# Performance work log

Hardware: AMD Instinct MI355X
Metric: run time of the kernel (lower is better)

Reference implementation:

```python
import jax, jax.numpy as jnp
import numpy as np

DIM = 10  # GMM components == feature dim


def _conv(x, w, b):
    y = jax.lax.conv_general_dilated(x, w, window_strides=(1, 1), padding='VALID',
                                     dimension_numbers=('NCHW', 'OIHW', 'NCHW'))
    return y + b[None, :, None, None]


def _gmm(x, centers, raw_mats):
    # x: [B, d]; centers: [K, d]; raw_mats: [K, d, d] with K == d == DIM
    K, d = centers.shape
    I = jnp.eye(d, dtype=x.dtype)
    L = jnp.tril(raw_mats, -1) + I                       # unit lower-triangular [K,d,d]
    root_D = jnp.diagonal(raw_mats, axis1=-2, axis2=-1)  # [K,d]
    D = root_D * root_D + 1e-4
    # Sigma_inv = L^{-T} D^{-1} L^{-1}
    L_inv = jax.scipy.linalg.solve_triangular(L, jnp.broadcast_to(I, L.shape), lower=True)
    Sigma_inv = jnp.einsum('kai,ka,kaj->kij', L_inv, 1.0 / D, L_inv)
    det_scale = jax.lax.rsqrt(jnp.prod(D, axis=-1))      # [K]
    diff = x[:, None, :] - centers[None, :, :]           # [B,K,d]
    dist_sq = jnp.einsum('bkd,kde,bke->bk', diff, Sigma_inv, diff)
    expo = -0.5 * dist_sq
    expo_safe = expo - jnp.max(expo, axis=1, keepdims=True)
    numer = det_scale[None, :] * jnp.exp(expo_safe)
    return numer / jnp.sum(numer, axis=1, keepdims=True)


def setup_inputs() -> dict:
    key = jax.random.key(0)
    ks = jax.random.split(key, 12)
    B = 4096
    x = jax.random.normal(ks[0], (B, 1, 28, 28), dtype=jnp.float32)
    conv1_w = jax.random.normal(ks[1], (32, 1, 3, 3), jnp.float32) * (1.0 / np.sqrt(1 * 9))
    conv1_b = jnp.zeros((32,), jnp.float32)
    conv2_w = jax.random.normal(ks[2], (64, 32, 3, 3), jnp.float32) * (1.0 / np.sqrt(32 * 9))
    conv2_b = jnp.zeros((64,), jnp.float32)
    fc1_w = jax.random.normal(ks[3], (128, 9216), jnp.float32) * (1.0 / np.sqrt(9216))
    fc1_b = jnp.zeros((128,), jnp.float32)
    fc2_w = jax.random.normal(ks[4], (DIM, 128), jnp.float32) * (1.0 / np.sqrt(128))
    fc2_b = jnp.zeros((DIM,), jnp.float32)
    centers = jax.random.normal(ks[5], (DIM, DIM), jnp.float32)
    raw_mats = jax.random.normal(ks[6], (DIM, DIM, DIM), jnp.float32) * 0.1 + jnp.eye(DIM)[None]
    return {'x': x, 'conv1_w': conv1_w, 'conv1_b': conv1_b, 'conv2_w': conv2_w,
            'conv2_b': conv2_b, 'fc1_w': fc1_w, 'fc1_b': fc1_b, 'fc2_w': fc2_w,
            'fc2_b': fc2_b, 'centers': centers, 'raw_mats': raw_mats}


def reference(x, conv1_w, conv1_b, conv2_w, conv2_b, fc1_w, fc1_b, fc2_w, fc2_b, centers, raw_mats):
    h = jax.nn.relu(_conv(x, conv1_w, conv1_b))          # [B,32,26,26]
    h = jax.nn.relu(_conv(h, conv2_w, conv2_b))          # [B,64,24,24]
    h = jax.lax.reduce_window(h, -jnp.inf, jax.lax.max, (1, 1, 2, 2), (1, 1, 2, 2), 'VALID')
    h = h.reshape(h.shape[0], -1)                        # [B,9216] (dropout = identity in eval)
    h = jax.nn.relu(h @ fc1_w.T + fc1_b)
    h = h @ fc2_w.T + fc2_b                              # [B,10]
    return _gmm(h, centers, raw_mats)
```

## Files before the change

### kernel.cpp

```cpp
#include <hip/hip_runtime.h>

typedef _Float16 half_t;
typedef _Float16 half8  __attribute__((ext_vector_type(8)));
typedef _Float16 half2v __attribute__((ext_vector_type(2)));
typedef float    floatx4 __attribute__((ext_vector_type(4)));
typedef float    float2v __attribute__((ext_vector_type(2)));

#define MFMA16(a, b, c) __builtin_amdgcn_mfma_f32_16x16x32_f16((a), (b), (c), 0, 0, 0)

__global__ void k_prep(const float* __restrict__ fw1, half_t* __restrict__ W1h,
                       const float* __restrict__ w2, half_t* __restrict__ W2T,
                       const float* __restrict__ raw, float* __restrict__ Sinv,
                       float* __restrict__ dets) {
    __shared__ float s_raw[1000];
    __shared__ float s_Li[1000];
    __shared__ float s_Dinv[100];
    const int blk = blockIdx.x;
    const int t = threadIdx.x;
    if (blk < 4608) {
        const int i = blk * 256 + t;
        W1h[i] = (half_t)fw1[i];
    } else if (blk < 4680) {
        const int i = (blk - 4608) * 256 + t;
        if (i < 18432) {
            const int tap = i / 2048;
            const int r = i - tap * 2048;
            const int co = r >> 5;
            const int ci = r & 31;
            W2T[i] = (half_t)w2[(co * 32 + ci) * 9 + tap];
        }
    } else {
        for (int i = t; i < 1000; i += 256) s_raw[i] = raw[i];
        __syncthreads();
        if (t < 100) {
            const int k = t / 10;
            const int j = t - k * 10;
            float v[10];
#pragma unroll
            for (int i = 0; i < 10; ++i) {
                float s = (i == j) ? 1.0f : 0.0f;
#pragma unroll
                for (int mm = 0; mm < 10; ++mm)
                    if (mm < i) s -= s_raw[k * 100 + i * 10 + mm] * v[mm];
                v[i] = s;
            }
#pragma unroll
            for (int a = 0; a < 10; ++a) s_Li[k * 100 + a * 10 + j] = v[a];
        } else if (t < 110) {
            const int k = t - 100;
            float prod = 1.0f;
#pragma unroll
            for (int a = 0; a < 10; ++a) {
                const float rd = s_raw[k * 100 + a * 10 + a];
                const float dv = rd * rd + 1e-4f;
                s_Dinv[k * 10 + a] = 1.0f / dv;
                prod *= dv;
            }
            dets[k] = rsqrtf(prod);
        }
        __syncthreads();
        for (int idx = t; idx < 1000; idx += 256) {
            const int k = idx / 100;
            const int r = idx - k * 100;
            const int ii = r / 10;
            const int jj = r - ii * 10;
            float s = 0.0f;
#pragma unroll
            for (int a = 0; a < 10; ++a)
                s += s_Li[k * 100 + a * 10 + ii] * s_Dinv[k * 10 + a] *
                     s_Li[k * 100 + a * 10 + jj];
            Sinv[idx] = s;
        }
    }
}

__global__ __launch_bounds__(256, 3) void k_convs(
    const float* __restrict__ x, const float* __restrict__ w1,
    const float* __restrict__ b1, const float* __restrict__ b2,
    const half_t* __restrict__ W2T, half_t* __restrict__ h2p) {
    __shared__ float s_x[784];
    __shared__ float s_w1[288];
    __shared__ float s_b1[32];
    __shared__ float s_b2[64];
    __shared__ __align__(16) half_t s_h1[688 * 32];

    const int t = threadIdx.x;
    const int b = blockIdx.x;

    for (int i = t; i < 784; i += 256) s_x[i] = x[(size_t)b * 784 + i];
    for (int i = t; i < 288; i += 256) s_w1[i] = w1[i];
    if (t < 32) s_b1[t] = b1[t];
    if (t < 64) s_b2[t] = b2[t];
    if (t < 48) {
        const int qq = t / 12;
        const int pp = 676 + (t - qq * 12);
        half8 z = {0, 0, 0, 0, 0, 0, 0, 0};
        *(half8*)((char*)s_h1 + (qq * 11008 + (pp << 4))) = z;
    }
    __syncthreads();

    const int w = t >> 6;
    const int ln = t & 63;
    const int n16 = ln & 15;
    const int q = ln >> 4;

    {
        float2v wr2[4][9], br2[4];
#pragma unroll
        for (int m = 0; m < 4; ++m) {
            br2[m][0] = s_b1[w * 8 + 2 * m];
            br2[m][1] = s_b1[w * 8 + 2 * m + 1];
#pragma unroll
            for (int k = 0; k < 9; ++k) {
                wr2[m][k][0] = s_w1[(w * 8 + 2 * m) * 9 + k];
                wr2[m][k][1] = s_w1[(w * 8 + 2 * m + 1) * 9 + k];
            }
        }
        for (int p = ln; p < 676; p += 64) {
            const int yy = p / 26;
            const int xx = p - yy * 26;
            float2v a2[4] = {br2[0], br2[1], br2[2], br2[3]};
#pragma unroll
            for (int r = 0; r < 3; ++r)
#pragma unroll
                for (int c = 0; c < 3; ++c) {
                    const float xv = s_x[(yy + r) * 28 + xx + c];
                    const float2v xv2 = {xv, xv};
#pragma unroll
                    for (int m = 0; m < 4; ++m)
                        a2[m] = xv2 * wr2[m][r * 3 + c] + a2[m];
                }
            half8 hv;
#pragma unroll
            for (int m = 0; m < 4; ++m) {
                hv[2 * m] = (half_t)fmaxf(a2[m][0], 0.0f);
                hv[2 * m + 1] = (half_t)fmaxf(a2[m][1], 0.0f);
            }
            *(half8*)((char*)s_h1 + (w * 11008 + (p << 4))) = hv;
        }
    }

    const int cp = w & 1;
    const int st = w >> 1;
    half8 bf[9][2];
#pragma unroll
    for (int tap = 0; tap < 9; ++tap)
#pragma unroll
        for (int cc = 0; cc < 2; ++cc)
            bf[tap][cc] = *(const half8*)(W2T +
                ((tap * 64 + (2 * cp + cc) * 16 + n16) * 32 + q * 8));

    __syncthreads();

#pragma unroll
    for (int tap = 0; tap < 9; ++tap)
#pragma unroll
        for (int cc = 0; cc < 2; ++cc)
            asm volatile("" : "+v"(bf[tap][cc]));

    const char* rp = (const char*)s_h1 + (q * 11008 + ((n16 + 16 * st) << 4));

    const float bb0 = s_b2[cp * 32 + n16];
    const float bb1 = s_b2[cp * 32 + 16 + n16];
    half_t* outp = h2p + (size_t)b * 9216 + (size_t)(cp * 32 + n16) * 144 +
                   8 * st + 2 * q;
    const bool dostore = (st == 0) | (q < 2);

    const floatx4 z4 = {0.f, 0.f, 0.f, 0.f};
    floatx4 sl0[2] = {z4, z4}, sl1[2] = {z4, z4}, sl2[2] = {z4, z4};
    float yb00 = 0.f, yb01 = 0.f, yb10 = 0.f, yb11 = 0.f;

#define RETIRE(YO, AC)                                                        \
    do {                                                                      \
        const float p0 = fmaxf(AC[0][0], AC[0][1]);                           \
        const float p1 = fmaxf(AC[0][2], AC[0][3]);                           \
        const float r0 = fmaxf(AC[1][0], AC[1][1]);                           \
        const float r1 = fmaxf(AC[1][2], AC[1][3]);                           \
        if (((YO) & 1) == 0) {                                                \
            yb00 = p0; yb01 = p1; yb10 = r0; yb11 = r1;                       \
        } else if (dostore) {                                                 \
            half2v h0, h1v;                                                   \
            h0[0] = (half_t)fmaxf(fmaxf(yb00, p0) + bb0, 0.0f);               \
            h0[1] = (half_t)fmaxf(fmaxf(yb01, p1) + bb0, 0.0f);               \
            h1v[0] = (half_t)fmaxf(fmaxf(yb10, r0) + bb1, 0.0f);              \
            h1v[1] = (half_t)fmaxf(fmaxf(yb11, r1) + bb1, 0.0f);              \
            half_t* op = outp + ((YO) >> 1) * 12;                             \
            *(half2v*)(op) = h0;                                              \
            *(half2v*)(op + 2304) = h1v;                                      \
        }                                                                     \
        AC[0] = z4; AC[1] = z4;                                               \
    } while (0)

#define CSTEP(Y_, A0, A1, A2)                                                 \
    do {                                                                      \
        const int y_ = (Y_);                                                  \
        if (y_ < 26) {                                                        \
            const half8 f0 = *(const half8*)(rp);                             \
            const half8 f1 = *(const half8*)(rp + 16);                        \
            const half8 f2 = *(const half8*)(rp + 32);                        \
            if (y_ <= 23) {                 \
                A0[0] = MFMA16(f0, bf[0][0], A0[0]);                          \
                A0[1] = MFMA16(f0, bf[0][1], A0[1]);                          \
                A0[0] = MFMA16(f1, bf[1][0], A0[0]);                          \
                A0[1] = MFMA16(f1, bf[1][1], A0[1]);                          \
                A0[0] = MFMA16(f2, bf[2][0], A0[0]);                          \
                A0[1] = MFMA16(f2, bf[2][1], A0[1]);                          \
            }                                                                 \
            if (y_ >= 1 && y_ <= 24) {    \
                A1[0] = MFMA16(f0, bf[3][0], A1[0]);                          \
                A1[1] = MFMA16(f0, bf[3][1], A1[1]);                          \
                A1[0] = MFMA16(f1, bf[4][0], A1[0]);                          \
                A1[1] = MFMA16(f1, bf[4][1], A1[1]);                          \
                A1[0] = MFMA16(f2, bf[5][0], A1[0]);                          \
                A1[1] = MFMA16(f2, bf[5][1], A1[1]);                          \
            }                                                                 \
            if (y_ >= 2) {   \
                A2[0] = MFMA16(f0, bf[6][0], A2[0]);                          \
                A2[1] = MFMA16(f0, bf[6][1], A2[1]);                          \
                A2[0] = MFMA16(f1, bf[7][0], A2[0]);                          \
                A2[1] = MFMA16(f1, bf[7][1], A2[1]);                          \
                A2[0] = MFMA16(f2, bf[8][0], A2[0]);                          \
                A2[1] = MFMA16(f2, bf[8][1], A2[1]);                          \
                RETIRE(y_ - 2, A2);                                           \
            }                                                                 \
            rp += 416;                                                        \
        }                                                                     \
    } while (0)

    for (int yb = 0; yb < 27; yb += 3) {
        CSTEP(yb + 0, sl0, sl2, sl1);
        CSTEP(yb + 1, sl1, sl0, sl2);
        CSTEP(yb + 2, sl2, sl1, sl0);
    }
#undef CSTEP
#undef RETIRE
}

__global__ __launch_bounds__(256) void k_fc1(const half_t* __restrict__ A,
                                             const half_t* __restrict__ W,
                                             half_t* __restrict__ part) {
    const int t = threadIdx.x;
    const int mb = blockIdx.x;
    const int kb = blockIdx.y;
    const int w = t >> 6, ln = t & 63, n16 = ln & 15, q = ln >> 4;

    const half_t* a0 = A + (size_t)(mb * 128 + w * 32 + n16) * 9216 + kb * 576 + q * 8;
    const half_t* a1 = a0 + (size_t)16 * 9216;
    const half_t* wp = W + (size_t)n16 * 9216 + kb * 576 + q * 8;

    floatx4 acc[2][8];
#pragma unroll
    for (int s = 0; s < 2; ++s)
#pragma unroll
        for (int nt = 0; nt < 8; ++nt) acc[s][nt] = (floatx4){0.f, 0.f, 0.f, 0.f};

#pragma unroll 2
    for (int kt = 0; kt < 18; ++kt) {
        const int ko = kt * 32;
        half8 af0 = *(const half8*)(a0 + ko);
        half8 af1 = *(const half8*)(a1 + ko);
#pragma unroll
        for (int nt = 0; nt < 8; ++nt) {
            half8 bfr = *(const half8*)(wp + (size_t)nt * 16 * 9216 + ko);
            acc[0][nt] = MFMA16(af0, bfr, acc[0][nt]);
            acc[1][nt] = MFMA16(af1, bfr, acc[1][nt]);
        }
    }
    const int rowbase = mb * 128 + w * 32;
#pragma unroll
    for (int s = 0; s < 2; ++s)
#pragma unroll
        for (int nt = 0; nt < 8; ++nt)
#pragma unroll
            for (int r = 0; r < 4; ++r) {
                const int row = rowbase + s * 16 + q * 4 + r;
                const int col = nt * 16 + n16;
                part[(size_t)kb * 524288 + (size_t)row * 128 + col] = (half_t)acc[s][nt][r];
            }
}

__global__ void k_fc1red(const half_t* __restrict__ part, const float* __restrict__ b,
                         half_t* __restrict__ h3) {
    const int idx = blockIdx.x * 256 + threadIdx.x;
    const int col = idx & 127;
    float s = 0.0f;
#pragma unroll
    for (int j = 0; j < 16; ++j) s += (float)part[(size_t)j * 524288 + idx];
    s = fmaxf(s + b[col], 0.0f);
    h3[idx] = (half_t)s;
}

__global__ __launch_bounds__(256) void k_fc2gmm(
    const half_t* __restrict__ h3, const float* __restrict__ fw,
    const float* __restrict__ fb, const float* __restrict__ cent,
    const float* __restrict__ Sinv, const float* __restrict__ dets,
    float* __restrict__ out) {
    __shared__ float sw[1280];
    __shared__ float sb[10];
    __shared__ float sc[100];
    __shared__ float ss[1000];
    __shared__ float sd[10];
    const int t = threadIdx.x;
    for (int i = t; i < 1280; i += 256) sw[i] = fw[i];
    if (t < 10) sb[t] = fb[t];
    if (t < 100) sc[t] = cent[t];
    for (int i = t; i < 1000; i += 256) ss[i] = Sinv[i];
    if (t < 10) sd[t] = dets[t];
    __syncthreads();

    const int bidx = blockIdx.x * 256 + t;
    half2v hh[64];
    const half2v* hp = (const half2v*)(h3 + (size_t)bidx * 128);
#pragma unroll
    for (int i = 0; i < 64; ++i) hh[i] = hp[i];

    float y[10];
#pragma unroll
    for (int o = 0; o < 10; ++o) {
        float a = sb[o];
#pragma unroll
        for (int k = 0; k < 64; ++k) {
            a = fmaf((float)hh[k][0], sw[o * 128 + 2 * k], a);
            a = fmaf((float)hh[k][1], sw[o * 128 + 2 * k + 1], a);
        }
        y[o] = a;
    }

    float expo[10];
    float mx = -3.402823466e38f;
#pragma unroll
    for (int k = 0; k < 10; ++k) {
        float d[10];
#pragma unroll
        for (int j = 0; j < 10; ++j) d[j] = y[j] - sc[k * 10 + j];
        float s = 0.0f;
#pragma unroll
        for (int i = 0; i < 10; ++i) {
            float r = 0.0f;
#pragma unroll
            for (int j = 0; j < 10; ++j) r = fmaf(ss[k * 100 + i * 10 + j], d[j], r);
            s = fmaf(d[i], r, s);
        }
        expo[k] = -0.5f * s;
        mx = fmaxf(mx, expo[k]);
    }
    float num[10];
    float sum = 0.0f;
#pragma unroll
    for (int k = 0; k < 10; ++k) {
        num[k] = sd[k] * __expf(expo[k] - mx);
        sum += num[k];
    }
    const float inv = 1.0f / sum;
#pragma unroll
    for (int k = 0; k < 10; ++k) out[(size_t)bidx * 10 + k] = num[k] * inv;
}

extern "C" void kernel_launch(void* const* d_in, const int* in_sizes, int n_in,
                              void* d_out, int out_size, void* d_ws, size_t ws_size,
                              hipStream_t stream) {
    const float* x = (const float*)d_in[0];
    const float* w1 = (const float*)d_in[1];
    const float* b1 = (const float*)d_in[2];
    const float* w2 = (const float*)d_in[3];
    const float* b2 = (const float*)d_in[4];
    const float* fw1 = (const float*)d_in[5];
    const float* fb1 = (const float*)d_in[6];
    const float* fw2 = (const float*)d_in[7];
    const float* fb2 = (const float*)d_in[8];
    const float* cen = (const float*)d_in[9];
    const float* raw = (const float*)d_in[10];
    float* out = (float*)d_out;

    char* ws = (char*)d_ws;
    half_t* W2T = (half_t*)(ws);
    half_t* W1h = (half_t*)(ws + 36864);
    half_t* h2p = (half_t*)(ws + 2396160);
    half_t* part = (half_t*)(ws + 77893632);
    half_t* h3h = (half_t*)(ws + 94670848);
    float* gS = (float*)(ws + 95719424);
    float* gD = (float*)(ws + 95723424);

    k_prep<<<4681, 256, 0, stream>>>(fw1, W1h, w2, W2T, raw, gS, gD);
    k_convs<<<4096, 256, 0, stream>>>(x, w1, b1, b2, W2T, h2p);
    k_fc1<<<dim3(32, 16), 256, 0, stream>>>(h2p, W1h, part);
    k_fc1red<<<2048, 256, 0, stream>>>(part, fb1, h3h);
    k_fc2gmm<<<16, 256, 0, stream>>>(h3h, fw2, fb2, cen, gS, gD, out);
}
```

Measured before the change: 247.0 us.

## Split conv rows across 8 waves and fuse fc1 reduction into GMM tail

The conv kernel now launches 512 threads per sample. Conv1 pixels are split across wave pairs, and the conv2 MFMA rows are split into two halves of 12 output rows, each handled by separate waves, which raises parallelism per block. The separate fc1 split-K reduction kernel is fused into the fc2+GMM kernel, which now sums the 16 partial slices directly and drops the intermediate h3 buffer and one launch. The tail kernel runs with only 64 blocks of 64 threads, so it may be latency bound, and the heavier conv blocks may lower occupancy.

```diff
diff --git a/kernel.cpp b/kernel.cpp
--- a/kernel.cpp
+++ b/kernel.cpp
@@ -74,7 +74,7 @@
     }
 }
 
-__global__ __launch_bounds__(256, 3) void k_convs(
+__global__ __launch_bounds__(512, 4) void k_convs(
     const float* __restrict__ x, const float* __restrict__ w1,
     const float* __restrict__ b1, const float* __restrict__ b2,
     const half_t* __restrict__ W2T, half_t* __restrict__ h2p) {
@@ -87,8 +87,8 @@
     const int t = threadIdx.x;
     const int b = blockIdx.x;
 
-    for (int i = t; i < 784; i += 256) s_x[i] = x[(size_t)b * 784 + i];
-    for (int i = t; i < 288; i += 256) s_w1[i] = w1[i];
+    for (int i = t; i < 784; i += 512) s_x[i] = x[(size_t)b * 784 + i];
+    if (t < 288) s_w1[t] = w1[t];
     if (t < 32) s_b1[t] = b1[t];
     if (t < 64) s_b2[t] = b2[t];
     if (t < 48) {
@@ -105,18 +105,19 @@
     const int q = ln >> 4;
 
     {
+        const int o = w >> 1;
         float2v wr2[4][9], br2[4];
 #pragma unroll
         for (int m = 0; m < 4; ++m) {
-            br2[m][0] = s_b1[w * 8 + 2 * m];
-            br2[m][1] = s_b1[w * 8 + 2 * m + 1];
+            br2[m][0] = s_b1[o * 8 + 2 * m];
+            br2[m][1] = s_b1[o * 8 + 2 * m + 1];
 #pragma unroll
             for (int k = 0; k < 9; ++k) {
-                wr2[m][k][0] = s_w1[(w * 8 + 2 * m) * 9 + k];
-                wr2[m][k][1] = s_w1[(w * 8 + 2 * m + 1) * 9 + k];
-            }
-        }
-        for (int p = ln; p < 676; p += 64) {
+                wr2[m][k][0] = s_w1[(o * 8 + 2 * m) * 9 + k];
+                wr2[m][k][1] = s_w1[(o * 8 + 2 * m + 1) * 9 + k];
+            }
+        }
+        for (int p = ln + (w & 1) * 64; p < 676; p += 128) {
             const int yy = p / 26;
             const int xx = p - yy * 26;
             float2v a2[4] = {br2[0], br2[1], br2[2], br2[3]};
@@ -136,12 +137,14 @@
                 hv[2 * m] = (half_t)fmaxf(a2[m][0], 0.0f);
                 hv[2 * m + 1] = (half_t)fmaxf(a2[m][1], 0.0f);
             }
-            *(half8*)((char*)s_h1 + (w * 11008 + (p << 4))) = hv;
+            *(half8*)((char*)s_h1 + (o * 11008 + (p << 4))) = hv;
         }
     }
 
     const int cp = w & 1;
-    const int st = w >> 1;
+    const int st = (w >> 1) & 1;
+    const int yh = w >> 2;
+
     half8 bf[9][2];
 #pragma unroll
     for (int tap = 0; tap < 9; ++tap)
@@ -158,12 +161,13 @@
         for (int cc = 0; cc < 2; ++cc)
             asm volatile("" : "+v"(bf[tap][cc]));
 
-    const char* rp = (const char*)s_h1 + (q * 11008 + ((n16 + 16 * st) << 4));
+    const char* rp = (const char*)s_h1 +
+                     (q * 11008 + ((yh * 312 + 16 * st + n16) << 4));
 
     const float bb0 = s_b2[cp * 32 + n16];
     const float bb1 = s_b2[cp * 32 + 16 + n16];
     half_t* outp = h2p + (size_t)b * 9216 + (size_t)(cp * 32 + n16) * 144 +
-                   8 * st + 2 * q;
+                   yh * 72 + 8 * st + 2 * q;
     const bool dostore = (st == 0) | (q < 2);
 
     const floatx4 z4 = {0.f, 0.f, 0.f, 0.f};
@@ -191,14 +195,13 @@
         AC[0] = z4; AC[1] = z4;                                               \
     } while (0)
 
-#define CSTEP(Y_, A0, A1, A2)                                                 \
+#define CSTEP(S_, A0, A1, A2)                                                 \
     do {                                                                      \
-        const int y_ = (Y_);                                                  \
-        if (y_ < 26) {                                                        \
+        if ((S_) < 14) {                                                      \
             const half8 f0 = *(const half8*)(rp);                             \
             const half8 f1 = *(const half8*)(rp + 16);                        \
             const half8 f2 = *(const half8*)(rp + 32);                        \
-            if (y_ <= 23) {                 \
+            if ((S_) <= 11) {              \
                 A0[0] = MFMA16(f0, bf[0][0], A0[0]);                          \
                 A0[1] = MFMA16(f0, bf[0][1], A0[1]);                          \
                 A0[0] = MFMA16(f1, bf[1][0], A0[0]);                          \
@@ -206,7 +209,7 @@
                 A0[0] = MFMA16(f2, bf[2][0], A0[0]);                          \
                 A0[1] = MFMA16(f2, bf[2][1], A0[1]);                          \
             }                                                                 \
-            if (y_ >= 1 && y_ <= 24) {    \
+            if ((S_) >= 1 && (S_) <= 12) {       \
                 A1[0] = MFMA16(f0, bf[3][0], A1[0]);                          \
                 A1[1] = MFMA16(f0, bf[3][1], A1[1]);                          \
                 A1[0] = MFMA16(f1, bf[4][0], A1[0]);                          \
@@ -214,20 +217,21 @@
                 A1[0] = MFMA16(f2, bf[5][0], A1[0]);                          \
                 A1[1] = MFMA16(f2, bf[5][1], A1[1]);                          \
             }                                                                 \
-            if (y_ >= 2) {   \
+            if ((S_) >= 2) {        \
                 A2[0] = MFMA16(f0, bf[6][0], A2[0]);                          \
                 A2[1] = MFMA16(f0, bf[6][1], A2[1]);                          \
                 A2[0] = MFMA16(f1, bf[7][0], A2[0]);                          \
                 A2[1] = MFMA16(f1, bf[7][1], A2[1]);                          \
                 A2[0] = MFMA16(f2, bf[8][0], A2[0]);                          \
                 A2[1] = MFMA16(f2, bf[8][1], A2[1]);                          \
-                RETIRE(y_ - 2, A2);                                           \
+                RETIRE((S_) - 2, A2);                                         \
             }                                                                 \
             rp += 416;                                                        \
         }                                                                     \
     } while (0)
 
-    for (int yb = 0; yb < 27; yb += 3) {
+#pragma unroll
+    for (int yb = 0; yb < 15; yb += 3) {
         CSTEP(yb + 0, sl0, sl2, sl1);
         CSTEP(yb + 1, sl1, sl0, sl2);
         CSTEP(yb + 2, sl2, sl1, sl0);
@@ -279,51 +283,56 @@
             }
 }
 
-__global__ void k_fc1red(const half_t* __restrict__ part, const float* __restrict__ b,
-                         half_t* __restrict__ h3) {
-    const int idx = blockIdx.x * 256 + threadIdx.x;
-    const int col = idx & 127;
-    float s = 0.0f;
-#pragma unroll
-    for (int j = 0; j < 16; ++j) s += (float)part[(size_t)j * 524288 + idx];
-    s = fmaxf(s + b[col], 0.0f);
-    h3[idx] = (half_t)s;
-}
-
-__global__ __launch_bounds__(256) void k_fc2gmm(
-    const half_t* __restrict__ h3, const float* __restrict__ fw,
-    const float* __restrict__ fb, const float* __restrict__ cent,
-    const float* __restrict__ Sinv, const float* __restrict__ dets,
-    float* __restrict__ out) {
+__global__ __launch_bounds__(64) void k_tail(
+    const half_t* __restrict__ part, const float* __restrict__ fb1,
+    const float* __restrict__ fw, const float* __restrict__ fb,
+    const float* __restrict__ cent, const float* __restrict__ Sinv,
+    const float* __restrict__ dets, float* __restrict__ out) {
     __shared__ float sw[1280];
+    __shared__ float sfb1[128];
     __shared__ float sb[10];
     __shared__ float sc[100];
     __shared__ float ss[1000];
     __shared__ float sd[10];
     const int t = threadIdx.x;
-    for (int i = t; i < 1280; i += 256) sw[i] = fw[i];
+    for (int i = t; i < 1280; i += 64) sw[i] = fw[i];
+    for (int i = t; i < 128; i += 64) sfb1[i] = fb1[i];
     if (t < 10) sb[t] = fb[t];
-    if (t < 100) sc[t] = cent[t];
-    for (int i = t; i < 1000; i += 256) ss[i] = Sinv[i];
+    for (int i = t; i < 100; i += 64) sc[i] = cent[i];
+    for (int i = t; i < 1000; i += 64) ss[i] = Sinv[i];
     if (t < 10) sd[t] = dets[t];
     __syncthreads();
 
-    const int bidx = blockIdx.x * 256 + t;
-    half2v hh[64];
-    const half2v* hp = (const half2v*)(h3 + (size_t)bidx * 128);
-#pragma unroll
-    for (int i = 0; i < 64; ++i) hh[i] = hp[i];
+    const int smp = blockIdx.x * 64 + t;
+    const half_t* ps = part + (size_t)smp * 128;
 
     float y[10];
 #pragma unroll
-    for (int o = 0; o < 10; ++o) {
-        float a = sb[o];
-#pragma unroll
-        for (int k = 0; k < 64; ++k) {
-            a = fmaf((float)hh[k][0], sw[o * 128 + 2 * k], a);
-            a = fmaf((float)hh[k][1], sw[o * 128 + 2 * k + 1], a);
-        }
-        y[o] = a;
+    for (int o = 0; o < 10; ++o) y[o] = sb[o];
+
+#pragma unroll
+    for (int g = 0; g < 4; ++g) {
+        float acc[32];
+#pragma unroll
+        for (int c = 0; c < 32; ++c) acc[c] = 0.0f;
+#pragma unroll
+        for (int kb = 0; kb < 16; ++kb) {
+            const half8* pk = (const half8*)(ps + (size_t)kb * 524288 + g * 32);
+#pragma unroll
+            for (int vv = 0; vv < 4; ++vv) {
+                const half8 v = pk[vv];
+#pragma unroll
+                for (int j = 0; j < 8; ++j) acc[vv * 8 + j] += (float)v[j];
+            }
+        }
+#pragma unroll
+        for (int c = 0; c < 32; ++c) {
+            const half_t hv = (half_t)fmaxf(acc[c] + sfb1[g * 32 + c], 0.0f);
+            const float hf = (float)hv;
+#pragma unroll
+            for (int o = 0; o < 10; ++o)
+                y[o] = fmaf(hf, sw[o * 128 + g * 32 + c], y[o]);
+        }
     }
 
     float expo[10];
@@ -353,7 +362,7 @@
     }
     const float inv = 1.0f / sum;
 #pragma unroll
-    for (int k = 0; k < 10; ++k) out[(size_t)bidx * 10 + k] = num[k] * inv;
+    for (int k = 0; k < 10; ++k) out[(size_t)smp * 10 + k] = num[k] * inv;
 }
 
 extern "C" void kernel_launch(void* const* d_in, const int* in_sizes, int n_in,
@@ -377,13 +386,11 @@
     half_t* W1h = (half_t*)(ws + 36864);
     half_t* h2p = (half_t*)(ws + 2396160);
     half_t* part = (half_t*)(ws + 77893632);
-    half_t* h3h = (half_t*)(ws + 94670848);
     float* gS = (float*)(ws + 95719424);
     float* gD = (float*)(ws + 95723424);
 
     k_prep<<<4681, 256, 0, stream>>>(fw1, W1h, w2, W2T, raw, gS, gD);
-    k_convs<<<4096, 256, 0, stream>>>(x, w1, b1, b2, W2T, h2p);
+    k_convs<<<4096, 512, 0, stream>>>(x, w1, b1, b2, W2T, h2p);
     k_fc1<<<dim3(32, 16), 256, 0, stream>>>(h2p, W1h, part);
-    k_fc1red<<<2048, 256, 0, stream>>>(part, fb1, h3h);
-    k_fc2gmm<<<16, 256, 0, stream>>>(h3h, fw2, fb2, cen, gS, gD, out);
-}
+    k_tail<<<64, 64, 0, stream>>>(part, fb1, fw2, fb2, cen, gS, gD, out);
+}
```

Measured after the change: 550.7 us. 123% more time.
